# Kernel tuning notes

Measured on AMD Instinct MI355X. Metric: run time of the kernel, lower is better.

Reference implementation:

```python
import jax, jax.numpy as jnp
import numpy as np

B, T, D_MODEL = 256, 512, 512
INPUT_LEN = 512
K, TOP_K = 5, 2
HIDDEN = 64
DOUT = 128


def _gelu(x):
    # torch nn.GELU default = exact erf form
    return jax.nn.gelu(x, approximate=False)


def _conv1d(x, w, b, stride, pad):
    # x: (B, Cin, L), w: (Cout, Cin, Kw)
    y = jax.lax.conv_general_dilated(
        x, w, window_strides=(stride,), padding=[(pad, pad)],
        dimension_numbers=('NCH', 'OIH', 'NCH'))
    return y + b[None, :, None]


def _mlp(z, w1, b1, w2, b2):
    return _gelu(z @ w1 + b1) @ w2 + b2


def _forward(hidden_states, raw_input,
             router_conv_w, router_conv_b, router_head_w, router_head_b,
             mp_w1, mp_b1, mp_w2, mp_b2,
             lt_w1, lt_b1, lt_w2, lt_b2,
             mx_w1, mx_b1, mx_w2, mx_b2,
             ap_attn_w, ap_attn_b, ap_w1, ap_b1, ap_w2, ap_b2,
             cv_conv_w, cv_conv_b, cv_out_w, cv_out_b):
    b = hidden_states.shape[0]
    # ---- router on RAW input ----
    x = raw_input[:, None, :]                               # (B,1,L)
    f = _gelu(_conv1d(x, router_conv_w, router_conv_b, 16, 8))  # (B,16,32)
    # AdaptiveAvgPool1d(4): 32 -> 4 exact bins of width 8, then flatten(1)
    f = f.reshape(b, 16, 4, 8).mean(axis=-1).reshape(b, 64)
    logits = f @ router_head_w + router_head_b              # (B,K)

    # ---- top-k sparse routing (dense-equivalent combine) ----
    topk_vals, topk_idx = jax.lax.top_k(logits, TOP_K)      # (B,top_k)
    w = jax.nn.softmax(topk_vals, axis=-1)                  # (B,top_k)
    gates = jnp.zeros((b, K), dtype=w.dtype).at[
        jnp.arange(b)[:, None], topk_idx].add(w)            # (B,K)

    h = hidden_states
    # Head 0: MeanPool
    out0 = _mlp(h.mean(axis=1), mp_w1, mp_b1, mp_w2, mp_b2)
    # Head 1: LastToken
    out1 = _mlp(h[:, -1, :], lt_w1, lt_b1, lt_w2, lt_b2)
    # Head 2: MaxPool
    out2 = _mlp(h.max(axis=1), mx_w1, mx_b1, mx_w2, mx_b2)
    # Head 3: AttentionPool
    a = jax.nn.softmax(h @ ap_attn_w + ap_attn_b, axis=1)   # (B,T,1)
    out3 = _mlp((h * a).sum(axis=1), ap_w1, ap_b1, ap_w2, ap_b2)
    # Head 4: Conv1dPool (k=8, s=4, p=2)
    z = _gelu(_conv1d(h.transpose(0, 2, 1), cv_conv_w, cv_conv_b, 4, 2))  # (B,64,L')
    out4 = z.mean(axis=2) @ cv_out_w + cv_out_b

    outs = jnp.stack([out0, out1, out2, out3, out4], axis=1)  # (B,K,DOUT)
    return (gates[:, :, None] * outs).sum(axis=1)             # (B,DOUT)


def setup_inputs() -> dict:
    key = jax.random.key(0)
    ks = jax.random.split(key, 32)
    rn = lambda k, s, sc: jax.random.normal(k, s, jnp.float32) * sc
    s_d = 1.0 / np.sqrt(D_MODEL)
    s_h = 1.0 / np.sqrt(HIDDEN)
    inp = {
        'hidden_states': jax.random.normal(ks[0], (B, T, D_MODEL), jnp.float32),
        'raw_input': jax.random.normal(ks[1], (B, INPUT_LEN), jnp.float32),
        'router_conv_w': rn(ks[2], (16, 1, 32), 1.0 / np.sqrt(32)),
        'router_conv_b': jnp.zeros((16,), jnp.float32),
        'router_head_w': rn(ks[3], (64, K), 1.0 / 8.0),
        'router_head_b': jnp.zeros((K,), jnp.float32),
        'mp_w1': rn(ks[4], (D_MODEL, HIDDEN), s_d), 'mp_b1': jnp.zeros((HIDDEN,), jnp.float32),
        'mp_w2': rn(ks[5], (HIDDEN, DOUT), s_h), 'mp_b2': jnp.zeros((DOUT,), jnp.float32),
        'lt_w1': rn(ks[6], (D_MODEL, HIDDEN), s_d), 'lt_b1': jnp.zeros((HIDDEN,), jnp.float32),
        'lt_w2': rn(ks[7], (HIDDEN, DOUT), s_h), 'lt_b2': jnp.zeros((DOUT,), jnp.float32),
        'mx_w1': rn(ks[8], (D_MODEL, HIDDEN), s_d), 'mx_b1': jnp.zeros((HIDDEN,), jnp.float32),
        'mx_w2': rn(ks[9], (HIDDEN, DOUT), s_h), 'mx_b2': jnp.zeros((DOUT,), jnp.float32),
        'ap_attn_w': rn(ks[10], (D_MODEL, 1), s_d), 'ap_attn_b': jnp.zeros((1,), jnp.float32),
        'ap_w1': rn(ks[11], (D_MODEL, HIDDEN), s_d), 'ap_b1': jnp.zeros((HIDDEN,), jnp.float32),
        'ap_w2': rn(ks[12], (HIDDEN, DOUT), s_h), 'ap_b2': jnp.zeros((DOUT,), jnp.float32),
        'cv_conv_w': rn(ks[13], (HIDDEN, D_MODEL, 8), 1.0 / np.sqrt(D_MODEL * 8)),
        'cv_conv_b': jnp.zeros((HIDDEN,), jnp.float32),
        'cv_out_w': rn(ks[14], (HIDDEN, DOUT), s_h), 'cv_out_b': jnp.zeros((DOUT,), jnp.float32),
    }
    return inp


def reference(hidden_states, raw_input,
              router_conv_w, router_conv_b, router_head_w, router_head_b,
              mp_w1, mp_b1, mp_w2, mp_b2,
              lt_w1, lt_b1, lt_w2, lt_b2,
              mx_w1, mx_b1, mx_w2, mx_b2,
              ap_attn_w, ap_attn_b, ap_w1, ap_b1, ap_w2, ap_b2,
              cv_conv_w, cv_conv_b, cv_out_w, cv_out_b):
    return _forward(hidden_states, raw_input,
                    router_conv_w, router_conv_b, router_head_w, router_head_b,
                    mp_w1, mp_b1, mp_w2, mp_b2,
                    lt_w1, lt_b1, lt_w2, lt_b2,
                    mx_w1, mx_b1, mx_w2, mx_b2,
                    ap_attn_w, ap_attn_b, ap_w1, ap_b1, ap_w2, ap_b2,
                    cv_conv_w, cv_conv_b, cv_out_w, cv_out_b)
```

## Files before the change

### kernel.cpp

```cpp
#include <hip/hip_runtime.h>
#include <cstdint>
#include <cstddef>


using short8   = short   __attribute__((ext_vector_type(8)));
using ushort4v = unsigned short __attribute__((ext_vector_type(4)));
using f32x4    = float   __attribute__((ext_vector_type(4)));

__device__ __forceinline__ unsigned short f2bf(float f) {
  unsigned int u = __float_as_uint(f);
  u += 0x7FFFu + ((u >> 16) & 1u);
  return (unsigned short)(u >> 16);
}
__device__ __forceinline__ float bf2f(unsigned short s) {
  return __uint_as_float((unsigned int)s << 16);
}
__device__ __forceinline__ float geluf(float x) {
  return 0.5f * x * (1.0f + erff(x * 0.7071067811865475f));
}

__global__ __launch_bounds__(256) void k_prep(const float* __restrict__ wcv,
                                              unsigned short* __restrict__ pB) {
  int flat = blockIdx.x * 256 + threadIdx.x;
  int jj   = flat & 7;
  int lane = (flat >> 3) & 63;
  int s    = (flat >> 9) & 127;
  int ot   = flat >> 16;
  int o = ot * 16 + (lane & 15);
  int k = s >> 4;
  int c = ((s & 15) << 5) + ((lane >> 4) << 3) + jj;
  pB[flat] = f2bf(wcv[(o * 512 + c) * 8 + k]);
}

__global__ __launch_bounds__(64) void k_router(
    const float* __restrict__ raw, const float* __restrict__ wc,
    const float* __restrict__ bc, const float* __restrict__ wh,
    const float* __restrict__ bh, float* __restrict__ gates) {
  __shared__ float xr[512];
  __shared__ float gbuf[512];
  __shared__ float f2[64];
  __shared__ float lg[5];
  int b = blockIdx.x, tid = threadIdx.x;
#pragma unroll
  for (int i = 0; i < 8; ++i) xr[tid + 64 * i] = raw[b * 512 + tid + 64 * i];
  __syncthreads();
  for (int u = 0; u < 8; ++u) {
    int oi = tid + 64 * u;
    int jf = oi >> 5, tp = oi & 31;
    float s = bc[jf];
    int base = 16 * tp - 8;
#pragma unroll
    for (int k = 0; k < 32; ++k) {
      int ix = base + k;
      if (ix >= 0 && ix < 512) s += xr[ix] * wc[jf * 32 + k];
    }
    gbuf[oi] = geluf(s);
  }
  __syncthreads();
  {
    int base = (tid >> 2) * 32 + (tid & 3) * 8;
    float acc = 0.0f;
#pragma unroll
    for (int u = 0; u < 8; ++u) acc += gbuf[base + u];
    f2[tid] = acc * 0.125f;
  }
  __syncthreads();
  if (tid < 5) {
    float s = bh[tid];
    for (int i = 0; i < 64; ++i) s += f2[i] * wh[i * 5 + tid];
    lg[tid] = s;
  }
  __syncthreads();
  if (tid == 0) {
    float v[5];
#pragma unroll
    for (int e = 0; e < 5; ++e) v[e] = lg[e];
    int i0 = 0;
    for (int e = 1; e < 5; ++e) if (v[e] > v[i0]) i0 = e;
    int i1 = -1;
    for (int e = 0; e < 5; ++e)
      if (e != i0 && (i1 < 0 || v[e] > v[i1])) i1 = e;
    float e1 = __expf(v[i1] - v[i0]);
    float w0 = 1.0f / (1.0f + e1);
    float g[5] = {0, 0, 0, 0, 0};
    g[i0] = w0; g[i1] = 1.0f - w0;
    for (int e = 0; e < 5; ++e) gates[b * 5 + e] = g[e];
  }
}

#define BUF_BYTES 69632
#define ZSCR_OFF  (2 * BUF_BYTES)
#define SC_OFF    (ZSCR_OFF + 2048 * 4)
#define PART_OFF  (SC_OFF + 68 * 4)
#define SMEM_MAIN (PART_OFF + 136 * 4)

__global__ __launch_bounds__(512, 2) void k_main(
    const float* __restrict__ h, const float* __restrict__ apw,
    const float* __restrict__ apb, const unsigned short* __restrict__ pB,
    const float* __restrict__ cvb, float* __restrict__ wsmean,
    float* __restrict__ wsmax, float* __restrict__ wsattn,
    float* __restrict__ wszm) {
  extern __shared__ char smem[];
  float* zscr = (float*)(smem + ZSCR_OFF);
  float* sc   = (float*)(smem + SC_OFF);
  float* part = (float*)(smem + PART_OFF);

  const int tid  = threadIdx.x;
  const int lane = tid & 63;
  const int wave = tid >> 6;
  const int b    = blockIdx.x;
  const float* hb = h + (size_t)b * 512 * 512;
  const int c4  = (tid & 127) << 2;
  const int myq = tid >> 7;

  float4 aw = *(const float4*)(apw + c4);
  const float apb0 = apb[0];
  float cvbv = (tid < 64) ? cvb[tid] : 0.0f;

  float s0 = 0, s1 = 0, s2 = 0, s3 = 0;
  float m0 = -3e38f, m1 = -3e38f, m2 = -3e38f, m3 = -3e38f;
  float o0 = 0, o1 = 0, o2 = 0, o3 = 0;
  float l_run = 0.0f, m_run = -1e30f;
  float zacc = 0.0f;

  auto stage_pool = [&](char* buf, float4 v, int tl) {
    int off = (tl << 10) + (c4 << 1);
    off ^= (off >> 8) & 0x70;
    ushort4v uv;
    uv[0] = f2bf(v.x); uv[1] = f2bf(v.y); uv[2] = f2bf(v.z); uv[3] = f2bf(v.w);
    *(ushort4v*)(buf + off) = uv;
    if (tl >= 2 && tl < 66) {
      s0 += v.x; s1 += v.y; s2 += v.z; s3 += v.w;
      m0 = fmaxf(m0, v.x); m1 = fmaxf(m1, v.y);
      m2 = fmaxf(m2, v.z); m3 = fmaxf(m3, v.w);
      float sp = v.x * aw.x + v.y * aw.y + v.z * aw.z + v.w * aw.w;
#pragma unroll
      for (int d = 1; d < 64; d <<= 1) sp += __shfl_xor(sp, d);
      if (lane == 0) part[tl * 2 + (wave & 1)] = sp;
    }
  };

  auto softmax_upd = [&](const char* buf) {
    float cmax = -1e30f;
    for (int r = 0; r < 64; ++r) cmax = fmaxf(cmax, sc[r + 2]);
    float mn = fmaxf(m_run, cmax);
    float scl = __expf(m_run - mn);
    o0 *= scl; o1 *= scl; o2 *= scl; o3 *= scl;
    l_run *= scl; m_run = mn;
#pragma unroll 4
    for (int r = 0; r < 64; ++r) {
      float e = __expf(sc[r + 2] - mn);
      l_run += e;
      if ((r & 3) == myq) {
        int off = ((r + 2) << 10) + (c4 << 1);
        off ^= (off >> 8) & 0x70;
        ushort4v hv = *(const ushort4v*)(buf + off);
        o0 += e * bf2f(hv[0]); o1 += e * bf2f(hv[1]);
        o2 += e * bf2f(hv[2]); o3 += e * bf2f(hv[3]);
      }
    }
  };

  auto conv_block = [&](const char* buf) {
    f32x4 acc = {0.0f, 0.0f, 0.0f, 0.0f};
    const int ot = wave & 3, kh = wave >> 2;
    const int pl = lane & 15, gg = lane >> 4;
#pragma unroll 4
    for (int si = 0; si < 64; ++si) {
      int s = kh * 64 + si;
      int k = s >> 4;
      int c0 = ((s & 15) << 5) + (gg << 3);
      int aoff = ((4 * pl + k) << 10) + (c0 << 1);
      aoff ^= (aoff >> 8) & 0x70;
      short8 av = *(const short8*)(buf + aoff);
      short8 bv = *(const short8*)(pB + ((size_t)((ot * 128 + s) * 64 + lane) << 3));
      acc = __builtin_amdgcn_mfma_f32_16x16x32_bf16(av, bv, acc, 0, 0, 0);
    }
    float* zs = zscr + kh * 1024;
#pragma unroll
    for (int r = 0; r < 4; ++r)
      zs[(gg * 4 + r) * 64 + ot * 16 + pl] = acc[r];
  };

  {
#pragma unroll
    for (int i = 0; i < 17; ++i) {
      int f = tid + 512 * i;
      int tl = f >> 7;
      int t = tl - 2;
      float4 v = make_float4(0.f, 0.f, 0.f, 0.f);
      if (t >= 0) v = *(const float4*)(hb + (size_t)t * 512 + c4);
      stage_pool(smem, v, tl);
    }
  }
  __syncthreads();
  if (tid < 64) sc[tid + 2] = part[(tid + 2) * 2] + part[(tid + 2) * 2 + 1] + apb0;
  __syncthreads();
  softmax_upd(smem);

  for (int j = 0; j < 8; ++j) {
    char* cur = smem + (j & 1) * BUF_BYTES;
    char* nxt = smem + ((j + 1) & 1) * BUF_BYTES;
    float4 pf[17];
    if (j < 7) {
#pragma unroll
      for (int i = 0; i < 17; ++i) {
        int f = tid + 512 * i;
        int tl = f >> 7;
        int t = 64 * (j + 1) - 2 + tl;
        pf[i] = make_float4(0.f, 0.f, 0.f, 0.f);
        if (t < 512) pf[i] = *(const float4*)(hb + (size_t)t * 512 + c4);
      }
    }
    conv_block(cur);
    __syncthreads();
    if (tid < 64) {
#pragma unroll 4
      for (int p = 0; p < 16; ++p) {
        float z = zscr[p * 64 + tid] + zscr[1024 + p * 64 + tid] + cvbv;
        zacc += geluf(z);
      }
    }
    __syncthreads();
    if (j < 7) {
#pragma unroll
      for (int i = 0; i < 17; ++i) {
        int f = tid + 512 * i;
        int tl = f >> 7;
        stage_pool(nxt, pf[i], tl);
      }
      __syncthreads();
      if (tid < 64) sc[tid + 2] = part[(tid + 2) * 2] + part[(tid + 2) * 2 + 1] + apb0;
      __syncthreads();
      softmax_upd(nxt);
    }
  }

  if (tid < 64) wszm[b * 64 + tid] = zacc * (1.0f / 128.0f);

  float invl = 1.0f / l_run;
  {
    float4 t4; t4.x = s0; t4.y = s1; t4.z = s2; t4.w = s3;
    *(float4*)(zscr + myq * 512 + c4) = t4;
    __syncthreads();
    if (tid < 128) {
      int c = tid << 2;
      float4 a = *(float4*)(zscr + c);
      float4 b4 = *(float4*)(zscr + 512 + c);
      float4 c4v = *(float4*)(zscr + 1024 + c);
      float4 d4 = *(float4*)(zscr + 1536 + c);
      float4 r;
      r.x = (a.x + b4.x + c4v.x + d4.x) * (1.0f / 512.0f);
      r.y = (a.y + b4.y + c4v.y + d4.y) * (1.0f / 512.0f);
      r.z = (a.z + b4.z + c4v.z + d4.z) * (1.0f / 512.0f);
      r.w = (a.w + b4.w + c4v.w + d4.w) * (1.0f / 512.0f);
      *(float4*)(wsmean + (size_t)b * 512 + c) = r;
    }
    __syncthreads();
  }
  {
    float4 t4; t4.x = m0; t4.y = m1; t4.z = m2; t4.w = m3;
    *(float4*)(zscr + myq * 512 + c4) = t4;
    __syncthreads();
    if (tid < 128) {
      int c = tid << 2;
      float4 a = *(float4*)(zscr + c);
      float4 b4 = *(float4*)(zscr + 512 + c);
      float4 c4v = *(float4*)(zscr + 1024 + c);
      float4 d4 = *(float4*)(zscr + 1536 + c);
      float4 r;
      r.x = fmaxf(fmaxf(a.x, b4.x), fmaxf(c4v.x, d4.x));
      r.y = fmaxf(fmaxf(a.y, b4.y), fmaxf(c4v.y, d4.y));
      r.z = fmaxf(fmaxf(a.z, b4.z), fmaxf(c4v.z, d4.z));
      r.w = fmaxf(fmaxf(a.w, b4.w), fmaxf(c4v.w, d4.w));
      *(float4*)(wsmax + (size_t)b * 512 + c) = r;
    }
    __syncthreads();
  }
  {
    float4 t4; t4.x = o0; t4.y = o1; t4.z = o2; t4.w = o3;
    *(float4*)(zscr + myq * 512 + c4) = t4;
    __syncthreads();
    if (tid < 128) {
      int c = tid << 2;
      float4 a = *(float4*)(zscr + c);
      float4 b4 = *(float4*)(zscr + 512 + c);
      float4 c4v = *(float4*)(zscr + 1024 + c);
      float4 d4 = *(float4*)(zscr + 1536 + c);
      float4 r;
      r.x = (a.x + b4.x + c4v.x + d4.x) * invl;
      r.y = (a.y + b4.y + c4v.y + d4.y) * invl;
      r.z = (a.z + b4.z + c4v.z + d4.z) * invl;
      r.w = (a.w + b4.w + c4v.w + d4.w) * invl;
      *(float4*)(wsattn + (size_t)b * 512 + c) = r;
    }
  }
}

__global__ __launch_bounds__(256) void k_epi(
    const float* __restrict__ h, const float* __restrict__ gates,
    const float* __restrict__ wsmean, const float* __restrict__ wsmax,
    const float* __restrict__ wsattn, const float* __restrict__ wszm,
    const float* __restrict__ mpw1, const float* __restrict__ mpb1,
    const float* __restrict__ mpw2, const float* __restrict__ mpb2,
    const float* __restrict__ ltw1, const float* __restrict__ ltb1,
    const float* __restrict__ ltw2, const float* __restrict__ ltb2,
    const float* __restrict__ mxw1, const float* __restrict__ mxb1,
    const float* __restrict__ mxw2, const float* __restrict__ mxb2,
    const float* __restrict__ apw1, const float* __restrict__ apb1,
    const float* __restrict__ apw2, const float* __restrict__ apb2,
    const float* __restrict__ cvow, const float* __restrict__ cvob,
    float* __restrict__ out) {
  __shared__ float xs[512];
  __shared__ float hp[256];
  __shared__ float h1[64];
  int b = blockIdx.x, tid = threadIdx.x;
  const int jj = tid & 63, qq = tid >> 6;
  float oacc = 0.0f;
#pragma unroll
  for (int br = 0; br < 4; ++br) {
    const float *w1, *b1, *w2, *b2, *xsrc;
    if (br == 0)      { w1 = mpw1; b1 = mpb1; w2 = mpw2; b2 = mpb2; xsrc = wsmean + (size_t)b * 512; }
    else if (br == 1) { w1 = ltw1; b1 = ltb1; w2 = ltw2; b2 = ltb2; xsrc = h + ((size_t)b * 512 + 511) * 512; }
    else if (br == 2) { w1 = mxw1; b1 = mxb1; w2 = mxw2; b2 = mxb2; xsrc = wsmax + (size_t)b * 512; }
    else              { w1 = apw1; b1 = apb1; w2 = apw2; b2 = apb2; xsrc = wsattn + (size_t)b * 512; }
    xs[tid] = xsrc[tid];
    xs[tid + 256] = xsrc[tid + 256];
    __syncthreads();
    float p = 0.0f;
    for (int c = qq * 128; c < qq * 128 + 128; ++c) p += xs[c] * w1[c * 64 + jj];
    hp[qq * 64 + jj] = p;
    __syncthreads();
    if (tid < 64)
      h1[tid] = geluf(hp[tid] + hp[64 + tid] + hp[128 + tid] + hp[192 + tid] + b1[tid]);
    __syncthreads();
    if (tid < 128) {
      float o = b2[tid];
      for (int hh = 0; hh < 64; ++hh) o += h1[hh] * w2[hh * 128 + tid];
      oacc += gates[b * 5 + br] * o;
    }
    __syncthreads();
  }
  if (tid < 64) h1[tid] = wszm[b * 64 + tid];
  __syncthreads();
  if (tid < 128) {
    float o = cvob[tid];
    for (int hh = 0; hh < 64; ++hh) o += h1[hh] * cvow[hh * 128 + tid];
    oacc += gates[b * 5 + 4] * o;
    out[b * 128 + tid] = oacc;
  }
}

extern "C" void kernel_launch(void* const* d_in, const int* in_sizes, int n_in,
                              void* d_out, int out_size, void* d_ws, size_t ws_size,
                              hipStream_t stream) {
  const float* h    = (const float*)d_in[0];
  const float* raw  = (const float*)d_in[1];
  const float* rcw  = (const float*)d_in[2];
  const float* rcb  = (const float*)d_in[3];
  const float* rhw  = (const float*)d_in[4];
  const float* rhb  = (const float*)d_in[5];
  const float* mpw1 = (const float*)d_in[6];
  const float* mpb1 = (const float*)d_in[7];
  const float* mpw2 = (const float*)d_in[8];
  const float* mpb2 = (const float*)d_in[9];
  const float* ltw1 = (const float*)d_in[10];
  const float* ltb1 = (const float*)d_in[11];
  const float* ltw2 = (const float*)d_in[12];
  const float* ltb2 = (const float*)d_in[13];
  const float* mxw1 = (const float*)d_in[14];
  const float* mxb1 = (const float*)d_in[15];
  const float* mxw2 = (const float*)d_in[16];
  const float* mxb2 = (const float*)d_in[17];
  const float* apw  = (const float*)d_in[18];
  const float* apb  = (const float*)d_in[19];
  const float* apw1 = (const float*)d_in[20];
  const float* apb1 = (const float*)d_in[21];
  const float* apw2 = (const float*)d_in[22];
  const float* apb2 = (const float*)d_in[23];
  const float* cvw  = (const float*)d_in[24];
  const float* cvbb = (const float*)d_in[25];
  const float* cvow = (const float*)d_in[26];
  const float* cvob = (const float*)d_in[27];

  char* ws = (char*)d_ws;
  float* gates  = (float*)(ws + 0);
  float* wszm   = (float*)(ws + 5120);
  float* wsmean = (float*)(ws + 70656);
  float* wsmax  = (float*)(ws + 594944);
  float* wsattn = (float*)(ws + 1119232);
  unsigned short* pB = (unsigned short*)(ws + 1643520);

  hipFuncSetAttribute((const void*)k_main,
                      hipFuncAttributeMaxDynamicSharedMemorySize, SMEM_MAIN);

  k_prep<<<1024, 256, 0, stream>>>(cvw, pB);
  k_router<<<256, 64, 0, stream>>>(raw, rcw, rcb, rhw, rhb, gates);
  k_main<<<256, 512, SMEM_MAIN, stream>>>(h, apw, apb, pB, cvbb,
                                          wsmean, wsmax, wsattn, wszm);
  k_epi<<<256, 256, 0, stream>>>(h, gates, wsmean, wsmax, wsattn, wszm,
                                 mpw1, mpb1, mpw2, mpb2, ltw1, ltb1, ltw2, ltb2,
                                 mxw1, mxb1, mxw2, mxb2, apw1, apb1, apw2, apb2,
                                 cvow, cvob, (float*)d_out);
}
```

Measured before the change: 585.8 us.

## Split each batch across two blocks and drop double buffering

Launches two blocks per batch element, each covering half of the sequence, and merges the partial sums, maxes and attention sums in the epilogue kernel. Removes the double-buffered staging and online-max softmax, using plain exp sums, so shared memory shrinks and occupancy rises. It also tweaks shuffle reductions and MFMA priority. The cost is extra epilogue reads and exposed load latency without prefetch, and exp without max subtraction could overflow for large attention scores.

```diff
diff --git a/kernel.cpp b/kernel.cpp
--- a/kernel.cpp
+++ b/kernel.cpp
@@ -88,219 +88,179 @@
   }
 }
 
-#define BUF_BYTES 69632
-#define ZSCR_OFF  (2 * BUF_BYTES)
-#define SC_OFF    (ZSCR_OFF + 2048 * 4)
-#define PART_OFF  (SC_OFF + 68 * 4)
-#define SMEM_MAIN (PART_OFF + 136 * 4)
-
-__global__ __launch_bounds__(512, 2) void k_main(
+#define ZSCR_OFF   69632
+#define PART_OFF   77824
+#define ESC_OFF    80272
+#define LPART_OFF  80528
+#define SMEM_MAIN  80544
+
+__global__ __launch_bounds__(512, 4) void k_main(
     const float* __restrict__ h, const float* __restrict__ apw,
     const float* __restrict__ apb, const unsigned short* __restrict__ pB,
-    const float* __restrict__ cvb, float* __restrict__ wsmean,
-    float* __restrict__ wsmax, float* __restrict__ wsattn,
+    const float* __restrict__ cvb,
+    float* __restrict__ wsmean, float* __restrict__ wsmax,
+    float* __restrict__ wsattn, float* __restrict__ wsl,
     float* __restrict__ wszm) {
   extern __shared__ char smem[];
-  float* zscr = (float*)(smem + ZSCR_OFF);
-  float* sc   = (float*)(smem + SC_OFF);
-  float* part = (float*)(smem + PART_OFF);
+  float* zscr  = (float*)(smem + ZSCR_OFF);
+  float* part  = (float*)(smem + PART_OFF);
+  float* esc   = (float*)(smem + ESC_OFF);
+  float* lpart = (float*)(smem + LPART_OFF);
 
   const int tid  = threadIdx.x;
   const int lane = tid & 63;
   const int wave = tid >> 6;
-  const int b    = blockIdx.x;
-  const float* hb = h + (size_t)b * 512 * 512;
-  const int c4  = (tid & 127) << 2;
-  const int myq = tid >> 7;
-
-  float4 aw = *(const float4*)(apw + c4);
+  const int bh   = blockIdx.x;
+  const int b    = bh >> 1;
+  const int half = bh & 1;
+  const float* hb = h + (size_t)b * 262144;
+  const int c4   = (tid & 127) << 2;
+  const int myq  = tid >> 7;
+
+  const float4 aw = *(const float4*)(apw + c4);
   const float apb0 = apb[0];
-  float cvbv = (tid < 64) ? cvb[tid] : 0.0f;
-
-  float s0 = 0, s1 = 0, s2 = 0, s3 = 0;
-  float m0 = -3e38f, m1 = -3e38f, m2 = -3e38f, m3 = -3e38f;
-  float o0 = 0, o1 = 0, o2 = 0, o3 = 0;
-  float l_run = 0.0f, m_run = -1e30f;
-  float zacc = 0.0f;
-
-  auto stage_pool = [&](char* buf, float4 v, int tl) {
-    int off = (tl << 10) + (c4 << 1);
-    off ^= (off >> 8) & 0x70;
-    ushort4v uv;
-    uv[0] = f2bf(v.x); uv[1] = f2bf(v.y); uv[2] = f2bf(v.z); uv[3] = f2bf(v.w);
-    *(ushort4v*)(buf + off) = uv;
-    if (tl >= 2 && tl < 66) {
-      s0 += v.x; s1 += v.y; s2 += v.z; s3 += v.w;
-      m0 = fmaxf(m0, v.x); m1 = fmaxf(m1, v.y);
-      m2 = fmaxf(m2, v.z); m3 = fmaxf(m3, v.w);
-      float sp = v.x * aw.x + v.y * aw.y + v.z * aw.z + v.w * aw.w;
-#pragma unroll
-      for (int d = 1; d < 64; d <<= 1) sp += __shfl_xor(sp, d);
-      if (lane == 0) part[tl * 2 + (wave & 1)] = sp;
-    }
-  };
-
-  auto softmax_upd = [&](const char* buf) {
-    float cmax = -1e30f;
-    for (int r = 0; r < 64; ++r) cmax = fmaxf(cmax, sc[r + 2]);
-    float mn = fmaxf(m_run, cmax);
-    float scl = __expf(m_run - mn);
-    o0 *= scl; o1 *= scl; o2 *= scl; o3 *= scl;
-    l_run *= scl; m_run = mn;
+  const int zp = tid >> 5;
+  const int zo = (tid & 31) << 1;
+  const float cvb0 = cvb[zo], cvb1 = cvb[zo + 1];
+
+  const int ot = wave & 3, kh = wave >> 2;
+  const int pl = lane & 15, gg = lane >> 4;
+
+  float s0=0.f,s1=0.f,s2=0.f,s3=0.f;
+  float m0=-3e38f,m1=-3e38f,m2=-3e38f,m3=-3e38f;
+  float o0=0.f,o1=0.f,o2=0.f,o3=0.f;
+  float lsum = 0.f;
+  float zacc0 = 0.f, zacc1 = 0.f;
+
+  for (int jw = 0; jw < 4; ++jw) {
+    const int j = half * 4 + jw;
+    const int tbase = 64 * j - 2;
+#pragma unroll
+    for (int i = 0; i < 17; ++i) {
+      const int tl = (tid >> 7) + 4 * i;
+      const int t  = tbase + tl;
+      float4 v = make_float4(0.f, 0.f, 0.f, 0.f);
+      if (t >= 0 && t < 512) v = *(const float4*)(hb + (size_t)t * 512 + c4);
+      int off = (tl << 10) + ((tid & 127) << 3);
+      off ^= ((off >> 12) & 7) << 4;
+      ushort4v uv;
+      uv[0]=f2bf(v.x); uv[1]=f2bf(v.y); uv[2]=f2bf(v.z); uv[3]=f2bf(v.w);
+      *(ushort4v*)(smem + off) = uv;
+      if (tl >= 2 && tl < 66) {
+        s0+=v.x; s1+=v.y; s2+=v.z; s3+=v.w;
+        m0=fmaxf(m0,v.x); m1=fmaxf(m1,v.y); m2=fmaxf(m2,v.z); m3=fmaxf(m3,v.w);
+        float sp = v.x*aw.x + v.y*aw.y + v.z*aw.z + v.w*aw.w;
+        sp += __shfl_xor(sp, 1); sp += __shfl_xor(sp, 2);
+        sp += __shfl_xor(sp, 4); sp += __shfl_xor(sp, 8);
+        if ((lane & 15) == 0) part[tl * 9 + ((tid & 127) >> 4)] = sp;
+      }
+    }
+    __syncthreads();
+    {
+      const int rr = tid >> 3, jj = tid & 7;
+      float p = part[(rr + 2) * 9 + jj];
+      p += __shfl_xor(p, 1); p += __shfl_xor(p, 2); p += __shfl_xor(p, 4);
+      if (jj == 0) esc[rr] = __expf(p + apb0);
+    }
+    {
+      f32x4 acc = {0.f, 0.f, 0.f, 0.f};
+      __builtin_amdgcn_s_setprio(1);
+#pragma unroll 8
+      for (int si = 0; si < 64; ++si) {
+        const int s = kh * 64 + si;
+        const int k = s >> 4;
+        int aoff = ((4 * pl + k) << 10) + ((s & 15) << 6) + (gg << 4);
+        aoff ^= ((aoff >> 12) & 7) << 4;
+        short8 av = *(const short8*)(smem + aoff);
+        short8 bv = *(const short8*)(pB + ((size_t)((ot * 128 + s) * 64 + lane) << 3));
+        acc = __builtin_amdgcn_mfma_f32_16x16x32_bf16(av, bv, acc, 0, 0, 0);
+      }
+      __builtin_amdgcn_s_setprio(0);
+      float* zs = zscr + kh * 1024;
+#pragma unroll
+      for (int r = 0; r < 4; ++r)
+        zs[(gg * 4 + r) * 64 + ot * 16 + pl] = acc[r];
+    }
+    __syncthreads();
 #pragma unroll 4
-    for (int r = 0; r < 64; ++r) {
-      float e = __expf(sc[r + 2] - mn);
-      l_run += e;
-      if ((r & 3) == myq) {
-        int off = ((r + 2) << 10) + (c4 << 1);
-        off ^= (off >> 8) & 0x70;
-        ushort4v hv = *(const ushort4v*)(buf + off);
-        o0 += e * bf2f(hv[0]); o1 += e * bf2f(hv[1]);
-        o2 += e * bf2f(hv[2]); o3 += e * bf2f(hv[3]);
-      }
-    }
-  };
-
-  auto conv_block = [&](const char* buf) {
-    f32x4 acc = {0.0f, 0.0f, 0.0f, 0.0f};
-    const int ot = wave & 3, kh = wave >> 2;
-    const int pl = lane & 15, gg = lane >> 4;
-#pragma unroll 4
-    for (int si = 0; si < 64; ++si) {
-      int s = kh * 64 + si;
-      int k = s >> 4;
-      int c0 = ((s & 15) << 5) + (gg << 3);
-      int aoff = ((4 * pl + k) << 10) + (c0 << 1);
-      aoff ^= (aoff >> 8) & 0x70;
-      short8 av = *(const short8*)(buf + aoff);
-      short8 bv = *(const short8*)(pB + ((size_t)((ot * 128 + s) * 64 + lane) << 3));
-      acc = __builtin_amdgcn_mfma_f32_16x16x32_bf16(av, bv, acc, 0, 0, 0);
-    }
-    float* zs = zscr + kh * 1024;
-#pragma unroll
-    for (int r = 0; r < 4; ++r)
-      zs[(gg * 4 + r) * 64 + ot * 16 + pl] = acc[r];
-  };
-
-  {
-#pragma unroll
-    for (int i = 0; i < 17; ++i) {
-      int f = tid + 512 * i;
-      int tl = f >> 7;
-      int t = tl - 2;
-      float4 v = make_float4(0.f, 0.f, 0.f, 0.f);
-      if (t >= 0) v = *(const float4*)(hb + (size_t)t * 512 + c4);
-      stage_pool(smem, v, tl);
-    }
-  }
-  __syncthreads();
-  if (tid < 64) sc[tid + 2] = part[(tid + 2) * 2] + part[(tid + 2) * 2 + 1] + apb0;
-  __syncthreads();
-  softmax_upd(smem);
-
-  for (int j = 0; j < 8; ++j) {
-    char* cur = smem + (j & 1) * BUF_BYTES;
-    char* nxt = smem + ((j + 1) & 1) * BUF_BYTES;
-    float4 pf[17];
-    if (j < 7) {
-#pragma unroll
-      for (int i = 0; i < 17; ++i) {
-        int f = tid + 512 * i;
-        int tl = f >> 7;
-        int t = 64 * (j + 1) - 2 + tl;
-        pf[i] = make_float4(0.f, 0.f, 0.f, 0.f);
-        if (t < 512) pf[i] = *(const float4*)(hb + (size_t)t * 512 + c4);
-      }
-    }
-    conv_block(cur);
-    __syncthreads();
-    if (tid < 64) {
-#pragma unroll 4
-      for (int p = 0; p < 16; ++p) {
-        float z = zscr[p * 64 + tid] + zscr[1024 + p * 64 + tid] + cvbv;
-        zacc += geluf(z);
-      }
-    }
-    __syncthreads();
-    if (j < 7) {
-#pragma unroll
-      for (int i = 0; i < 17; ++i) {
-        int f = tid + 512 * i;
-        int tl = f >> 7;
-        stage_pool(nxt, pf[i], tl);
-      }
-      __syncthreads();
-      if (tid < 64) sc[tid + 2] = part[(tid + 2) * 2] + part[(tid + 2) * 2 + 1] + apb0;
-      __syncthreads();
-      softmax_upd(nxt);
-    }
-  }
-
-  if (tid < 64) wszm[b * 64 + tid] = zacc * (1.0f / 128.0f);
-
-  float invl = 1.0f / l_run;
-  {
-    float4 t4; t4.x = s0; t4.y = s1; t4.z = s2; t4.w = s3;
-    *(float4*)(zscr + myq * 512 + c4) = t4;
-    __syncthreads();
-    if (tid < 128) {
-      int c = tid << 2;
-      float4 a = *(float4*)(zscr + c);
-      float4 b4 = *(float4*)(zscr + 512 + c);
-      float4 c4v = *(float4*)(zscr + 1024 + c);
-      float4 d4 = *(float4*)(zscr + 1536 + c);
-      float4 r;
-      r.x = (a.x + b4.x + c4v.x + d4.x) * (1.0f / 512.0f);
-      r.y = (a.y + b4.y + c4v.y + d4.y) * (1.0f / 512.0f);
-      r.z = (a.z + b4.z + c4v.z + d4.z) * (1.0f / 512.0f);
-      r.w = (a.w + b4.w + c4v.w + d4.w) * (1.0f / 512.0f);
-      *(float4*)(wsmean + (size_t)b * 512 + c) = r;
-    }
-    __syncthreads();
-  }
-  {
-    float4 t4; t4.x = m0; t4.y = m1; t4.z = m2; t4.w = m3;
-    *(float4*)(zscr + myq * 512 + c4) = t4;
-    __syncthreads();
-    if (tid < 128) {
-      int c = tid << 2;
-      float4 a = *(float4*)(zscr + c);
-      float4 b4 = *(float4*)(zscr + 512 + c);
-      float4 c4v = *(float4*)(zscr + 1024 + c);
-      float4 d4 = *(float4*)(zscr + 1536 + c);
-      float4 r;
-      r.x = fmaxf(fmaxf(a.x, b4.x), fmaxf(c4v.x, d4.x));
-      r.y = fmaxf(fmaxf(a.y, b4.y), fmaxf(c4v.y, d4.y));
-      r.z = fmaxf(fmaxf(a.z, b4.z), fmaxf(c4v.z, d4.z));
-      r.w = fmaxf(fmaxf(a.w, b4.w), fmaxf(c4v.w, d4.w));
-      *(float4*)(wsmax + (size_t)b * 512 + c) = r;
-    }
-    __syncthreads();
-  }
-  {
-    float4 t4; t4.x = o0; t4.y = o1; t4.z = o2; t4.w = o3;
-    *(float4*)(zscr + myq * 512 + c4) = t4;
-    __syncthreads();
-    if (tid < 128) {
-      int c = tid << 2;
-      float4 a = *(float4*)(zscr + c);
-      float4 b4 = *(float4*)(zscr + 512 + c);
-      float4 c4v = *(float4*)(zscr + 1024 + c);
-      float4 d4 = *(float4*)(zscr + 1536 + c);
-      float4 r;
-      r.x = (a.x + b4.x + c4v.x + d4.x) * invl;
-      r.y = (a.y + b4.y + c4v.y + d4.y) * invl;
-      r.z = (a.z + b4.z + c4v.z + d4.z) * invl;
-      r.w = (a.w + b4.w + c4v.w + d4.w) * invl;
-      *(float4*)(wsattn + (size_t)b * 512 + c) = r;
-    }
+    for (int u = 0; u < 16; ++u) {
+      const int r = u * 4 + myq;
+      const float e = esc[r];
+      lsum += e;
+      int off = ((r + 2) << 10) + ((tid & 127) << 3);
+      off ^= ((off >> 12) & 7) << 4;
+      ushort4v hv = *(const ushort4v*)(smem + off);
+      o0 += e * bf2f(hv[0]); o1 += e * bf2f(hv[1]);
+      o2 += e * bf2f(hv[2]); o3 += e * bf2f(hv[3]);
+    }
+    {
+      float2 za = *(const float2*)(zscr + zp * 64 + zo);
+      float2 zb = *(const float2*)(zscr + 1024 + zp * 64 + zo);
+      zacc0 += geluf(za.x + zb.x + cvb0);
+      zacc1 += geluf(za.y + zb.y + cvb1);
+    }
+    __syncthreads();
+  }
+
+  float* red = (float*)smem;
+  if ((tid & 127) == 0) lpart[myq] = lsum;
+  *(float4*)(red + myq * 512 + c4) = make_float4(s0, s1, s2, s3);
+  __syncthreads();
+  if (tid < 128) {
+    const int c = tid << 2;
+    float4 a = *(float4*)(red + c);
+    float4 b4 = *(float4*)(red + 512 + c);
+    float4 cc = *(float4*)(red + 1024 + c);
+    float4 d4 = *(float4*)(red + 1536 + c);
+    *(float4*)(wsmean + (size_t)bh * 512 + c) =
+        make_float4(a.x+b4.x+cc.x+d4.x, a.y+b4.y+cc.y+d4.y,
+                    a.z+b4.z+cc.z+d4.z, a.w+b4.w+cc.w+d4.w);
+  }
+  if (tid == 0) wsl[bh] = lpart[0] + lpart[1] + lpart[2] + lpart[3];
+  __syncthreads();
+  *(float4*)(red + myq * 512 + c4) = make_float4(m0, m1, m2, m3);
+  __syncthreads();
+  if (tid < 128) {
+    const int c = tid << 2;
+    float4 a = *(float4*)(red + c);
+    float4 b4 = *(float4*)(red + 512 + c);
+    float4 cc = *(float4*)(red + 1024 + c);
+    float4 d4 = *(float4*)(red + 1536 + c);
+    *(float4*)(wsmax + (size_t)bh * 512 + c) =
+        make_float4(fmaxf(fmaxf(a.x,b4.x), fmaxf(cc.x,d4.x)),
+                    fmaxf(fmaxf(a.y,b4.y), fmaxf(cc.y,d4.y)),
+                    fmaxf(fmaxf(a.z,b4.z), fmaxf(cc.z,d4.z)),
+                    fmaxf(fmaxf(a.w,b4.w), fmaxf(cc.w,d4.w)));
+  }
+  __syncthreads();
+  *(float4*)(red + myq * 512 + c4) = make_float4(o0, o1, o2, o3);
+  __syncthreads();
+  if (tid < 128) {
+    const int c = tid << 2;
+    float4 a = *(float4*)(red + c);
+    float4 b4 = *(float4*)(red + 512 + c);
+    float4 cc = *(float4*)(red + 1024 + c);
+    float4 d4 = *(float4*)(red + 1536 + c);
+    *(float4*)(wsattn + (size_t)bh * 512 + c) =
+        make_float4(a.x+b4.x+cc.x+d4.x, a.y+b4.y+cc.y+d4.y,
+                    a.z+b4.z+cc.z+d4.z, a.w+b4.w+cc.w+d4.w);
+  }
+  __syncthreads();
+  *(float2*)(red + zp * 64 + zo) = make_float2(zacc0, zacc1);
+  __syncthreads();
+  if (tid < 64) {
+    float s = 0.f;
+#pragma unroll
+    for (int p = 0; p < 16; ++p) s += red[p * 64 + tid];
+    wszm[bh * 64 + tid] = s;
   }
 }
 
 __global__ __launch_bounds__(256) void k_epi(
     const float* __restrict__ h, const float* __restrict__ gates,
     const float* __restrict__ wsmean, const float* __restrict__ wsmax,
-    const float* __restrict__ wsattn, const float* __restrict__ wszm,
+    const float* __restrict__ wsattn, const float* __restrict__ wsl,
+    const float* __restrict__ wszm,
     const float* __restrict__ mpw1, const float* __restrict__ mpb1,
     const float* __restrict__ mpw2, const float* __restrict__ mpb2,
     const float* __restrict__ ltw1, const float* __restrict__ ltb1,
@@ -316,16 +276,29 @@
   __shared__ float h1[64];
   int b = blockIdx.x, tid = threadIdx.x;
   const int jj = tid & 63, qq = tid >> 6;
+  const float invL = 1.0f / (wsl[2 * b] + wsl[2 * b + 1]);
   float oacc = 0.0f;
 #pragma unroll
   for (int br = 0; br < 4; ++br) {
-    const float *w1, *b1, *w2, *b2, *xsrc;
-    if (br == 0)      { w1 = mpw1; b1 = mpb1; w2 = mpw2; b2 = mpb2; xsrc = wsmean + (size_t)b * 512; }
-    else if (br == 1) { w1 = ltw1; b1 = ltb1; w2 = ltw2; b2 = ltb2; xsrc = h + ((size_t)b * 512 + 511) * 512; }
-    else if (br == 2) { w1 = mxw1; b1 = mxb1; w2 = mxw2; b2 = mxb2; xsrc = wsmax + (size_t)b * 512; }
-    else              { w1 = apw1; b1 = apb1; w2 = apw2; b2 = apb2; xsrc = wsattn + (size_t)b * 512; }
-    xs[tid] = xsrc[tid];
-    xs[tid + 256] = xsrc[tid + 256];
+    const float *w1, *b1, *w2, *b2;
+    if (br == 0)      { w1 = mpw1; b1 = mpb1; w2 = mpw2; b2 = mpb2; }
+    else if (br == 1) { w1 = ltw1; b1 = ltb1; w2 = ltw2; b2 = ltb2; }
+    else if (br == 2) { w1 = mxw1; b1 = mxb1; w2 = mxw2; b2 = mxb2; }
+    else              { w1 = apw1; b1 = apb1; w2 = apw2; b2 = apb2; }
+#pragma unroll
+    for (int u = 0; u < 2; ++u) {
+      int idx = tid + 256 * u;
+      float v;
+      if (br == 0)
+        v = (wsmean[(size_t)(2*b)*512+idx] + wsmean[(size_t)(2*b+1)*512+idx]) * (1.0f/512.0f);
+      else if (br == 1)
+        v = h[((size_t)b * 512 + 511) * 512 + idx];
+      else if (br == 2)
+        v = fmaxf(wsmax[(size_t)(2*b)*512+idx], wsmax[(size_t)(2*b+1)*512+idx]);
+      else
+        v = (wsattn[(size_t)(2*b)*512+idx] + wsattn[(size_t)(2*b+1)*512+idx]) * invL;
+      xs[idx] = v;
+    }
     __syncthreads();
     float p = 0.0f;
     for (int c = qq * 128; c < qq * 128 + 128; ++c) p += xs[c] * w1[c * 64 + jj];
@@ -341,7 +314,8 @@
     }
     __syncthreads();
   }
-  if (tid < 64) h1[tid] = wszm[b * 64 + tid];
+  if (tid < 64)
+    h1[tid] = (wszm[(2*b)*64 + tid] + wszm[(2*b+1)*64 + tid]) * (1.0f / 128.0f);
   __syncthreads();
   if (tid < 128) {
     float o = cvob[tid];
@@ -385,20 +359,21 @@
 
   char* ws = (char*)d_ws;
   float* gates  = (float*)(ws + 0);
-  float* wszm   = (float*)(ws + 5120);
-  float* wsmean = (float*)(ws + 70656);
-  float* wsmax  = (float*)(ws + 594944);
-  float* wsattn = (float*)(ws + 1119232);
-  unsigned short* pB = (unsigned short*)(ws + 1643520);
+  float* wsl    = (float*)(ws + 8192);
+  float* wszm   = (float*)(ws + 16384);
+  float* wsmean = (float*)(ws + 262144);
+  float* wsmax  = (float*)(ws + 1310720);
+  float* wsattn = (float*)(ws + 2359296);
+  unsigned short* pB = (unsigned short*)(ws + 3407872);
 
   hipFuncSetAttribute((const void*)k_main,
                       hipFuncAttributeMaxDynamicSharedMemorySize, SMEM_MAIN);
 
   k_prep<<<1024, 256, 0, stream>>>(cvw, pB);
   k_router<<<256, 64, 0, stream>>>(raw, rcw, rcb, rhw, rhb, gates);
-  k_main<<<256, 512, SMEM_MAIN, stream>>>(h, apw, apb, pB, cvbb,
-                                          wsmean, wsmax, wsattn, wszm);
-  k_epi<<<256, 256, 0, stream>>>(h, gates, wsmean, wsmax, wsattn, wszm,
+  k_main<<<512, 512, SMEM_MAIN, stream>>>(h, apw, apb, pB, cvbb,
+                                          wsmean, wsmax, wsattn, wsl, wszm);
+  k_epi<<<256, 256, 0, stream>>>(h, gates, wsmean, wsmax, wsattn, wsl, wszm,
                                  mpw1, mpb1, mpw2, mpb2, ltw1, ltb1, ltw2, ltb2,
                                  mxw1, mxb1, mxw2, mxb2, apw1, apb1, apw2, apb2,
                                  cvow, cvob, (float*)d_out);
```

Result: faster. 547.4 us (-6.6%).
